# Kernel optimization log

Hardware: AMD Instinct MI355X
Metric: run time of the kernel (lower is better)

The kernel has to match this reference:

```python
import jax, jax.numpy as jnp
import numpy as np

LAYERS = [2048, 2048, 2048, 512]
THRESHOLD = 1.0
TAU_MEM = 20.0
TAU_SYN = 5.0
DT = 1.0
BATCH = 32
T = 100


def setup_inputs() -> dict:
    key = jax.random.key(0)
    ks = jax.random.split(key, 2 + 2 * (len(LAYERS) - 1))
    inp = {
        "x": jax.random.uniform(ks[0], (BATCH, LAYERS[0]), dtype=jnp.float32),
        "noise": jax.random.uniform(ks[1], (T, BATCH, LAYERS[0]), dtype=jnp.float32),
        "time_steps": T,
    }
    # nn.Linear-style init: U(-1/sqrt(fan_in), 1/sqrt(fan_in))
    for i in range(len(LAYERS) - 1):
        fan_in, fan_out = LAYERS[i], LAYERS[i + 1]
        bound = 1.0 / np.sqrt(fan_in)
        inp[f"W{i}"] = jax.random.uniform(ks[2 + 2 * i], (fan_out, fan_in), minval=-bound, maxval=bound, dtype=jnp.float32)
        inp[f"b{i}"] = jax.random.uniform(ks[3 + 2 * i], (fan_out,), minval=-bound, maxval=bound, dtype=jnp.float32)
    return inp


def _lif_step(I, mem, syn):
    # dI_syn/dt = -I_syn/tau_syn + I ; dV/dt = -V/tau_mem + I_syn  (explicit Euler, dt=1)
    syn = syn + (-syn / TAU_SYN + I) * DT
    mem = mem + (-mem / TAU_MEM + syn) * DT
    spikes = (mem >= THRESHOLD).astype(mem.dtype)
    mem = mem * (1.0 - spikes)          # reset fired neurons
    mem = mem * (mem > 0).astype(mem.dtype)  # clamp negative potentials to 0
    return spikes, mem, syn


def reference(x, noise, W0, b0, W1, b1, W2, b2, time_steps):
    params = [(W0, b0), (W1, b1), (W2, b2)]
    batch = x.shape[0]
    dtype = x.dtype
    rate = jnp.clip(x, 0.0, 1.0)                       # [B, in]
    in_spikes = (noise < rate[None]).astype(dtype)     # [T, B, in] Poisson encoding

    mems = tuple(jnp.zeros((batch, W.shape[0]), dtype) for W, _ in params)
    syns = tuple(jnp.zeros((batch, W.shape[0]), dtype) for W, _ in params)

    def step(carry, sp_in):
        mems, syns = carry
        layer_in = sp_in
        new_mems, new_syns = [], []
        count = jnp.zeros((), dtype)
        for (W, b), m, s in zip(params, mems, syns):
            I = layer_in @ W.T + b
            spk, m, s = _lif_step(I, m, s)
            new_mems.append(m)
            new_syns.append(s)
            count = count + spk.sum()
            layer_in = spk
        return (tuple(new_mems), tuple(new_syns)), (layer_in, count)

    (_, _), (out_spikes, counts) = jax.lax.scan(step, (mems, syns), in_spikes)
    output = out_spikes.mean(axis=0)   # [B, out]: time-averaged output spike train
    total_spikes = counts.sum()
    return output, total_spikes
```

## Files before the change

kernel.cpp:

```cpp
#include <hip/hip_runtime.h>
#include <hip/hip_cooperative_groups.h>

#define T_STEPS 100
#define MTOT    3200
#define R0_OFF  0
#define R1_OFF  13107200
#define I_OFF   26214400

typedef _Float16 half8_t __attribute__((ext_vector_type(8)));
typedef _Float16 half4_t __attribute__((ext_vector_type(4)));
typedef float    f32x4   __attribute__((ext_vector_type(4)));

__device__ __forceinline__ void encode512_body(
    int blk, const float* __restrict__ x, const float* __restrict__ noise,
    _Float16* __restrict__ spk0, float* __restrict__ out, _Float16* smem)
{
    if (blk == 0 && threadIdx.x == 0) out[16384] = 0.0f;
    const int tid  = threadIdx.x;
    const int m0   = blk * 16;
    const int koct = tid & 255;
    const int mlh  = tid >> 8;
    half8_t* lds = (half8_t*)smem;
    #pragma unroll
    for (int mlq = 0; mlq < 8; ++mlq) {
        const int ml = mlq * 2 + mlh;
        const int m  = m0 + ml;
        const int t = m >> 5, b = m & 31;
        const float4 x1 = *(const float4*)(x + b * 2048 + koct * 8);
        const float4 x2 = *(const float4*)(x + b * 2048 + koct * 8 + 4);
        const float4 n1 = *(const float4*)(noise + (size_t)t * 65536 + b * 2048 + koct * 8);
        const float4 n2 = *(const float4*)(noise + (size_t)t * 65536 + b * 2048 + koct * 8 + 4);
        const float xr[8] = {x1.x,x1.y,x1.z,x1.w,x2.x,x2.y,x2.z,x2.w};
        const float nz[8] = {n1.x,n1.y,n1.z,n1.w,n2.x,n2.y,n2.z,n2.w};
        half8_t sp;
        #pragma unroll
        for (int q = 0; q < 8; ++q) {
            const float r = fminf(fmaxf(xr[q], 0.0f), 1.0f);
            sp[q] = (nz[q] < r) ? (_Float16)1.0f : (_Float16)0.0f;
        }
        lds[ml * 256 + (koct ^ ml)] = sp;
    }
    __syncthreads();
    #pragma unroll
    for (int r = 0; r < 8; ++r) {
        const int ml  = tid & 15;
        const int oct = r * 32 + (tid >> 4);
        *(half8_t*)(spk0 + ((size_t)oct * MTOT + m0 + ml) * 8)
            = lds[ml * 256 + (oct ^ ml)];
    }
}

__device__ __forceinline__ void convw512_body(
    int cblk, const float* __restrict__ W, _Float16* __restrict__ Wf)
{
    const int koct = threadIdx.x & 255;
    const int rh   = threadIdx.x >> 8;
    #pragma unroll
    for (int r = 0; r < 8; ++r) {
        const int row = cblk * 16 + rh * 8 + r;
        const float* wp = W + (size_t)row * 2048 + koct * 8;
        const float4 f1 = *(const float4*)(wp);
        const float4 f2 = *(const float4*)(wp + 4);
        half8_t h = {(_Float16)f1.x,(_Float16)f1.y,(_Float16)f1.z,(_Float16)f1.w,
                     (_Float16)f2.x,(_Float16)f2.y,(_Float16)f2.z,(_Float16)f2.w};
        const size_t idx = (size_t)(row >> 4) * 32768
                         + ((size_t)((koct >> 2) * 64 + (koct & 3) * 16 + (row & 15))) * 8;
        *(half8_t*)(Wf + idx) = h;
    }
}

__device__ __forceinline__ void scan512_body(
    int blk, const _Float16* __restrict__ I, const float* __restrict__ bias,
    _Float16* __restrict__ spk_out, float* __restrict__ out,
    const int is_last, float* rsum)
{
    const int gid = blk * 512 + threadIdx.x;
    const int j   = gid & 7;
    const int b   = (gid >> 3) & 31;
    const int oct = gid >> 8;
    const int n   = oct * 8 + j;
    const float bi = bias[n];
    const size_t nbase = (size_t)oct * (MTOT * 8) + j;
    float mem = 0.f, syn = 0.f, osum = 0.f, cnt = 0.f;
    #pragma unroll 4
    for (int t = 0; t < T_STEPS; ++t) {
        const int m = t * 32 + b;
        const float Iv = (float)I[nbase + (size_t)m * 8] + bi;
        syn = syn + (-syn / 5.0f + Iv);
        mem = mem + (-mem / 20.0f + syn);
        const float sv = (mem >= 1.0f) ? 1.0f : 0.0f;
        mem = (sv != 0.0f) ? 0.0f : mem;
        mem = (mem > 0.0f) ? mem : 0.0f;
        cnt += sv; osum += sv;
        if (!is_last) spk_out[nbase + (size_t)m * 8] = (_Float16)sv;
    }
    if (is_last) out[b * 512 + n] = osum * 0.01f;
    float c = cnt;
    #pragma unroll
    for (int s2 = 1; s2 < 64; s2 <<= 1) c += __shfl_xor(c, s2);
    const int wid = threadIdx.x >> 6;
    if ((threadIdx.x & 63) == 0) rsum[wid] = c;
    __syncthreads();
    if (threadIdx.x == 0) {
        float s = rsum[0];
        #pragma unroll
        for (int ww = 1; ww < 8; ++ww) s += rsum[ww];
        atomicAdd(&out[16384], s);
    }
    __syncthreads();
}

__device__ __forceinline__ half8_t ldB(const _Float16* __restrict__ p, int kq) {
    return *(const half8_t*)(p + (size_t)kq * (MTOT * 8));
}

__device__ __forceinline__ void stage_q(
    const _Float16* __restrict__ Wf, _Float16* __restrict__ wlds,
    const int nbb, const int q, const int w, const int lane)
{
    #pragma unroll
    for (int r = 0; r < 8; ++r) {
        const int unit = r * 512 + w * 64 + lane;
        const int s = unit >> 10, off = unit & 1023;
        const _Float16* src = Wf + (size_t)(4 * nbb + s) * 32768
                            + (size_t)q * 8192 + (size_t)off * 8;
        _Float16* dst = wlds + (size_t)unit * 8;
        __builtin_amdgcn_global_load_lds(
            (const __attribute__((address_space(1))) void*)src,
            (__attribute__((address_space(3))) void*)dst, 16, 0, 0);
    }
}

template<bool HAS2>
__device__ __forceinline__ void kstep512(
    const _Float16* __restrict__ wlds, const _Float16* const (&bp)[2],
    half8_t (&bb)[2], f32x4 (&acc)[2][4],
    const int lane, const int quad, const int kb, const int j)
{
    half8_t a[4];
    #pragma unroll
    for (int s = 0; s < 4; ++s)
        a[s] = *(const half8_t*)(wlds + (size_t)s * 8192 + (size_t)(j * 64 + lane) * 8);
    #pragma unroll
    for (int s = 0; s < 4; ++s) {
        acc[0][s] = __builtin_amdgcn_mfma_f32_16x16x32_f16(a[s], bb[0], acc[0][s], 0, 0, 0);
        if (HAS2)
            acc[1][s] = __builtin_amdgcn_mfma_f32_16x16x32_f16(a[s], bb[1], acc[1][s], 0, 0, 0);
    }
    if (kb + 4 < 64) {
        const int kq = (kb + 4) * 4 + quad;
        bb[0] = ldB(bp[0], kq);
        if (HAS2) bb[1] = ldB(bp[1], kq);
    }
}

template<bool HAS2>
__device__ __forceinline__ void gemm64s_run(
    const _Float16* __restrict__ Wf, const _Float16* __restrict__ spk,
    _Float16* __restrict__ I, _Float16* __restrict__ wlds,
    const int (&mt)[2], const int nbb, const int row_base,
    const int w, const int lane, const int quad, const int mi,
    const bool st)
{
    const _Float16* bp[2];
    bp[0] = spk + ((size_t)mt[0] * 16 + mi) * 8;
    bp[1] = spk + ((size_t)mt[1] * 16 + mi) * 8;

    half8_t B0[2], B1[2], B2[2], B3[2];
    B0[0] = ldB(bp[0],      quad);
    B1[0] = ldB(bp[0],  4 + quad);
    B2[0] = ldB(bp[0],  8 + quad);
    B3[0] = ldB(bp[0], 12 + quad);
    if (HAS2) {
        B0[1] = ldB(bp[1],      quad);
        B1[1] = ldB(bp[1],  4 + quad);
        B2[1] = ldB(bp[1],  8 + quad);
        B3[1] = ldB(bp[1], 12 + quad);
    }

    stage_q(Wf, wlds, nbb, 0, w, lane);
    __syncthreads();

    f32x4 acc[2][4];
    #pragma unroll
    for (int u = 0; u < 2; ++u) {
        #pragma unroll
        for (int s = 0; s < 4; ++s) acc[u][s] = (f32x4){0, 0, 0, 0};
    }

    #pragma unroll 1
    for (int q = 0; q < 4; ++q) {
        #pragma unroll
        for (int j = 0; j < 16; j += 4) {
            kstep512<HAS2>(wlds, bp, B0, acc, lane, quad, q * 16 + j,     j);
            kstep512<HAS2>(wlds, bp, B1, acc, lane, quad, q * 16 + j + 1, j + 1);
            kstep512<HAS2>(wlds, bp, B2, acc, lane, quad, q * 16 + j + 2, j + 2);
            kstep512<HAS2>(wlds, bp, B3, acc, lane, quad, q * 16 + j + 3, j + 3);
        }
        __syncthreads();
        if (q < 3) {
            stage_q(Wf, wlds, nbb, q + 1, w, lane);
            __syncthreads();
        }
    }

    #pragma unroll
    for (int s = 0; s < 4; ++s) {
        const int n0 = row_base + s * 16 + quad * 4;
        const size_t obase = (size_t)(n0 >> 3) * (MTOT * 8) + (n0 & 7);
        #pragma unroll
        for (int u = 0; u < 2; ++u) {
            if (u == 0 && !st) continue;
            if (u == 1 && !HAS2) continue;
            half4_t h;
            #pragma unroll
            for (int r = 0; r < 4; ++r) h[r] = (_Float16)acc[u][s][r];
            *(half4_t*)(I + obase + (size_t)(mt[u] * 16 + mi) * 8) = h;
        }
    }
}

template<int NCHUNK>
__device__ __forceinline__ void gemm64s_body(
    const int bid, const _Float16* __restrict__ Wf,
    const _Float16* __restrict__ spk, _Float16* __restrict__ I,
    _Float16* __restrict__ wlds)
{
    const int tid  = threadIdx.x;
    const int lane = tid & 63;
    const int w    = tid >> 6;
    const int mi   = lane & 15;
    const int quad = lane >> 4;
    const int chunk = bid % NCHUNK;
    const int rest  = bid / NCHUNK;
    const int msl   = rest & 1;
    const int nbb   = rest >> 1;
    const int row_base = nbb * 64;
    const int jt     = (200 - chunk + NCHUNK - 1) / NCHUNK;
    const int jh     = (jt + 1) >> 1;
    const int jbase  = msl ? jh : 0;
    const int jcount = msl ? (jt - jh) : jh;
    const int rem    = jcount - 8;
    const bool has2  = (w < rem);
    const int r2     = rem > 0 ? rem : 0;
    const bool st    = has2 || (w + r2) < jcount;
    int jl_start = jbase + (has2 ? 2 * w : w + r2);
    const int jmax = jbase + jcount - 1;
    if (jl_start > jmax) jl_start = jmax;

    int mt[2];
    #pragma unroll
    for (int u = 0; u < 2; ++u) {
        int jl = jl_start + u;
        if (jl > jmax) jl = jmax;
        mt[u] = chunk + NCHUNK * jl;
    }

    if (has2) gemm64s_run<true >(Wf, spk, I, wlds, mt, nbb, row_base, w, lane, quad, mi, true);
    else      gemm64s_run<false>(Wf, spk, I, wlds, mt, nbb, row_base, w, lane, quad, mi, st);
}

__global__ __launch_bounds__(512, 4) void snn_mega_kernel(
    const float* __restrict__ x, const float* __restrict__ noise,
    const float* __restrict__ W0, const float* __restrict__ b0,
    const float* __restrict__ W1, const float* __restrict__ b1,
    const float* __restrict__ W2, const float* __restrict__ b2,
    _Float16* __restrict__ R0, _Float16* __restrict__ R1,
    _Float16* __restrict__ Ib, float* __restrict__ out)
{
    cooperative_groups::grid_group grid = cooperative_groups::this_grid();
    __shared__ _Float16 smem[32768];
    const int blk = blockIdx.x;

    if (blk < 200)      encode512_body(blk, x, noise, R0, out, smem);
    else if (blk < 328) convw512_body(blk - 200, W0, R1);
    grid.sync();
    gemm64s_body<8>(blk, R1, R0, Ib, smem);
    grid.sync();
    if (blk < 128)      scan512_body(blk, Ib, b0, R1, out, 0, (float*)smem);
    else if (blk < 256) convw512_body(blk - 128, W1, R0);
    grid.sync();
    gemm64s_body<8>(blk, R0, R1, Ib, smem);
    grid.sync();
    if (blk < 128)      scan512_body(blk, Ib, b1, R0, out, 0, (float*)smem);
    else if (blk < 160) convw512_body(blk - 128, W2, R1);
    grid.sync();
    if (blk < 256) gemm64s_body<16>(blk, R1, R0, Ib, smem);
    grid.sync();
    if (blk < 32) scan512_body(blk, Ib, b2, nullptr, out, 1, (float*)smem);
}

__global__ __launch_bounds__(512, 4) void snn_enc512_kernel(
    const float* __restrict__ x, const float* __restrict__ noise,
    _Float16* __restrict__ spk0, float* __restrict__ out,
    const float* __restrict__ W, _Float16* __restrict__ Wf)
{
    __shared__ _Float16 smem[32768];
    if (blockIdx.x < 200) encode512_body(blockIdx.x, x, noise, spk0, out, smem);
    else                  convw512_body(blockIdx.x - 200, W, Wf);
}

__global__ __launch_bounds__(512, 4) void snn_scan_convw512_kernel(
    const _Float16* __restrict__ I, const float* __restrict__ bias,
    _Float16* __restrict__ spk_out, float* __restrict__ out,
    const int scan_blocks, const float* __restrict__ W,
    _Float16* __restrict__ Wf)
{
    __shared__ float rsum[8];
    if ((int)blockIdx.x < scan_blocks)
        scan512_body(blockIdx.x, I, bias, spk_out, out, 0, rsum);
    else
        convw512_body(blockIdx.x - scan_blocks, W, Wf);
}

__global__ __launch_bounds__(512, 4) void snn_scan512_kernel(
    const _Float16* __restrict__ I, const float* __restrict__ bias,
    float* __restrict__ out)
{
    __shared__ float rsum[8];
    scan512_body(blockIdx.x, I, bias, nullptr, out, 1, rsum);
}

template<int NCHUNK>
__global__ __launch_bounds__(512, 4) void snn_gemm64s_kernel(
    const _Float16* __restrict__ Wf, const _Float16* __restrict__ spk,
    _Float16* __restrict__ I)
{
    __shared__ _Float16 wlds[32768];
    gemm64s_body<NCHUNK>(blockIdx.x, Wf, spk, I, wlds);
}

extern "C" void kernel_launch(void* const* d_in, const int* in_sizes, int n_in,
                              void* d_out, int out_size, void* d_ws, size_t ws_size,
                              hipStream_t stream) {
    const float* x     = (const float*)d_in[0];
    const float* noise = (const float*)d_in[1];
    const float* W0 = (const float*)d_in[3];
    const float* b0 = (const float*)d_in[4];
    const float* W1 = (const float*)d_in[5];
    const float* b1 = (const float*)d_in[6];
    const float* W2 = (const float*)d_in[7];
    const float* b2 = (const float*)d_in[8];
    float* out = (float*)d_out;

    _Float16* R0 = (_Float16*)((char*)d_ws + R0_OFF);
    _Float16* R1 = (_Float16*)((char*)d_ws + R1_OFF);
    _Float16* Ib = (_Float16*)((char*)d_ws + I_OFF);

    int maxb = 0;
    hipError_t oe = hipOccupancyMaxActiveBlocksPerMultiprocessor(
        &maxb, (const void*)snn_mega_kernel, 512, 0);

    if (oe == hipSuccess && maxb >= 2) {
        void* args[] = {(void*)&x, (void*)&noise,
                        (void*)&W0, (void*)&b0, (void*)&W1, (void*)&b1,
                        (void*)&W2, (void*)&b2,
                        (void*)&R0, (void*)&R1, (void*)&Ib, (void*)&out};
        hipLaunchCooperativeKernel((const void*)snn_mega_kernel,
                                   dim3(512), dim3(512), args, 0, stream);
    } else {
        snn_enc512_kernel<<<dim3(328), dim3(512), 0, stream>>>(x, noise, R0, out, W0, R1);
        snn_gemm64s_kernel<8><<<dim3(512), dim3(512), 0, stream>>>(R1, R0, Ib);
        snn_scan_convw512_kernel<<<dim3(256), dim3(512), 0, stream>>>(Ib, b0, R1, out, 128, W1, R0);
        snn_gemm64s_kernel<8><<<dim3(512), dim3(512), 0, stream>>>(R0, R1, Ib);
        snn_scan_convw512_kernel<<<dim3(160), dim3(512), 0, stream>>>(Ib, b1, R0, out, 128, W2, R1);
        snn_gemm64s_kernel<16><<<dim3(256), dim3(512), 0, stream>>>(R1, R0, Ib);
        snn_scan512_kernel<<<dim3(32), dim3(512), 0, stream>>>(Ib, b2, out);
    }

    (void)in_sizes; (void)n_in; (void)out_size; (void)ws_size;
}
```

Before: 245.7 us.

## Replace cooperative grid.sync with custom sharded atomic barriers and MFMA priority hints

Swaps the six cooperative-groups grid syncs for a hand-rolled barrier that spreads arrival counters over 8 cache-line-separated slots and uses a per-launch invocation counter to derive monotonically increasing targets, so the counters never need resetting. It also raises wave priority around the MFMA block and adds empty asm register constraints to pin B-operand loads in place. The goal is lower barrier latency and better MFMA issue. The barrier relies on relaxed atomics plus fences and assumes exactly 512 resident blocks, which is fragile if the grid size changes.

```diff
diff --git a/kernel.cpp b/kernel.cpp
--- a/kernel.cpp
+++ b/kernel.cpp
@@ -10,6 +10,28 @@
 typedef _Float16 half8_t __attribute__((ext_vector_type(8)));
 typedef _Float16 half4_t __attribute__((ext_vector_type(4)));
 typedef float    f32x4   __attribute__((ext_vector_type(4)));
+
+__device__ int g_inv;
+__device__ __attribute__((aligned(1024))) int g_bar[6][128];
+
+__device__ __forceinline__ void gate(const int p, const int target) {
+    __syncthreads();
+    if (threadIdx.x == 0) {
+        __threadfence();
+        __hip_atomic_fetch_add(&g_bar[p][(blockIdx.x & 7) * 16], 1,
+                               __ATOMIC_RELAXED, __HIP_MEMORY_SCOPE_AGENT);
+    }
+    if (threadIdx.x < 8) {
+        while (__hip_atomic_load(&g_bar[p][threadIdx.x * 16],
+                                 __ATOMIC_RELAXED, __HIP_MEMORY_SCOPE_AGENT)
+               < target) {
+            __builtin_amdgcn_s_sleep(1);
+        }
+    }
+    __syncthreads();
+    __threadfence();
+    __syncthreads();
+}
 
 __device__ __forceinline__ void encode512_body(
     int blk, const float* __restrict__ x, const float* __restrict__ noise,
@@ -48,6 +70,7 @@
         *(half8_t*)(spk0 + ((size_t)oct * MTOT + m0 + ml) * 8)
             = lds[ml * 256 + (oct ^ ml)];
     }
+    __syncthreads();
 }
 
 __device__ __forceinline__ void convw512_body(
@@ -141,16 +164,22 @@
     #pragma unroll
     for (int s = 0; s < 4; ++s)
         a[s] = *(const half8_t*)(wlds + (size_t)s * 8192 + (size_t)(j * 64 + lane) * 8);
+    __builtin_amdgcn_s_setprio(1);
     #pragma unroll
     for (int s = 0; s < 4; ++s) {
         acc[0][s] = __builtin_amdgcn_mfma_f32_16x16x32_f16(a[s], bb[0], acc[0][s], 0, 0, 0);
         if (HAS2)
             acc[1][s] = __builtin_amdgcn_mfma_f32_16x16x32_f16(a[s], bb[1], acc[1][s], 0, 0, 0);
     }
+    __builtin_amdgcn_s_setprio(0);
     if (kb + 4 < 64) {
         const int kq = (kb + 4) * 4 + quad;
         bb[0] = ldB(bp[0], kq);
-        if (HAS2) bb[1] = ldB(bp[1], kq);
+        asm volatile("" : "+v"(bb[0]));
+        if (HAS2) {
+            bb[1] = ldB(bp[1], kq);
+            asm volatile("" : "+v"(bb[1]));
+        }
     }
 }
 
@@ -171,11 +200,13 @@
     B1[0] = ldB(bp[0],  4 + quad);
     B2[0] = ldB(bp[0],  8 + quad);
     B3[0] = ldB(bp[0], 12 + quad);
+    asm volatile("" : "+v"(B0[0]), "+v"(B1[0]), "+v"(B2[0]), "+v"(B3[0]));
     if (HAS2) {
         B0[1] = ldB(bp[1],      quad);
         B1[1] = ldB(bp[1],  4 + quad);
         B2[1] = ldB(bp[1],  8 + quad);
         B3[1] = ldB(bp[1], 12 + quad);
+        asm volatile("" : "+v"(B0[1]), "+v"(B1[1]), "+v"(B2[1]), "+v"(B3[1]));
     }
 
     stage_q(Wf, wlds, nbb, 0, w, lane);
@@ -268,25 +299,33 @@
     _Float16* __restrict__ R0, _Float16* __restrict__ R1,
     _Float16* __restrict__ Ib, float* __restrict__ out)
 {
-    cooperative_groups::grid_group grid = cooperative_groups::this_grid();
     __shared__ _Float16 smem[32768];
+    __shared__ int s_k;
     const int blk = blockIdx.x;
+
+    if (threadIdx.x == 0) {
+        const int v = __hip_atomic_fetch_add(&g_inv, 1, __ATOMIC_RELAXED,
+                                             __HIP_MEMORY_SCOPE_AGENT);
+        s_k = (v >> 9) + 1;
+    }
+    __syncthreads();
+    const int tgt = 64 * s_k;
 
     if (blk < 200)      encode512_body(blk, x, noise, R0, out, smem);
     else if (blk < 328) convw512_body(blk - 200, W0, R1);
-    grid.sync();
+    gate(0, tgt);
     gemm64s_body<8>(blk, R1, R0, Ib, smem);
-    grid.sync();
+    gate(1, tgt);
     if (blk < 128)      scan512_body(blk, Ib, b0, R1, out, 0, (float*)smem);
     else if (blk < 256) convw512_body(blk - 128, W1, R0);
-    grid.sync();
+    gate(2, tgt);
     gemm64s_body<8>(blk, R0, R1, Ib, smem);
-    grid.sync();
+    gate(3, tgt);
     if (blk < 128)      scan512_body(blk, Ib, b1, R0, out, 0, (float*)smem);
     else if (blk < 160) convw512_body(blk - 128, W2, R1);
-    grid.sync();
+    gate(4, tgt);
     if (blk < 256) gemm64s_body<16>(blk, R1, R0, Ib, smem);
-    grid.sync();
+    gate(5, tgt);
     if (blk < 32) scan512_body(blk, Ib, b2, nullptr, out, 1, (float*)smem);
 }
 
```

Measured after the change: 298.3 us. 1.21x slower.

## Convert all weights upfront and prestage next-layer weights into LDS during scan

Applied to the files above, without the earlier changes.

When the workspace is large enough, the W1 and W2 fp32-to-fp16 conversions move into the first phase, using otherwise idle blocks and separate workspace buffers. During each scan phase, every block also preloads its first quarter of the next layer's weight tile into LDS, so the following GEMM skips its initial staging load and barrier. The aim is to take the weight-conversion work and the first LDS fill off the critical path between grid syncs. The cost is more workspace memory and a dependence on ws_size, and the scan's use of shared memory has to coexist with the prestaged tile in the same LDS buffer.

```diff
diff --git a/kernel.cpp b/kernel.cpp
--- a/kernel.cpp
+++ b/kernel.cpp
@@ -6,6 +6,9 @@
 #define R0_OFF  0
 #define R1_OFF  13107200
 #define I_OFF   26214400
+#define W1F_OFF 39321600
+#define W2F_OFF 47710208
+#define WS_CONS 49807360ULL
 
 typedef _Float16 half8_t __attribute__((ext_vector_type(8)));
 typedef _Float16 half4_t __attribute__((ext_vector_type(4)));
@@ -48,6 +51,7 @@
         *(half8_t*)(spk0 + ((size_t)oct * MTOT + m0 + ml) * 8)
             = lds[ml * 256 + (oct ^ ml)];
     }
+    __syncthreads();
 }
 
 __device__ __forceinline__ void convw512_body(
@@ -154,7 +158,7 @@
     }
 }
 
-template<bool HAS2>
+template<bool HAS2, bool PRE>
 __device__ __forceinline__ void gemm64s_run(
     const _Float16* __restrict__ Wf, const _Float16* __restrict__ spk,
     _Float16* __restrict__ I, _Float16* __restrict__ wlds,
@@ -178,8 +182,10 @@
         B3[1] = ldB(bp[1], 12 + quad);
     }
 
-    stage_q(Wf, wlds, nbb, 0, w, lane);
-    __syncthreads();
+    if (!PRE) {
+        stage_q(Wf, wlds, nbb, 0, w, lane);
+        __syncthreads();
+    }
 
     f32x4 acc[2][4];
     #pragma unroll
@@ -220,7 +226,7 @@
     }
 }
 
-template<int NCHUNK>
+template<int NCHUNK, bool PRE>
 __device__ __forceinline__ void gemm64s_body(
     const int bid, const _Float16* __restrict__ Wf,
     const _Float16* __restrict__ spk, _Float16* __restrict__ I,
@@ -256,8 +262,8 @@
         mt[u] = chunk + NCHUNK * jl;
     }
 
-    if (has2) gemm64s_run<true >(Wf, spk, I, wlds, mt, nbb, row_base, w, lane, quad, mi, true);
-    else      gemm64s_run<false>(Wf, spk, I, wlds, mt, nbb, row_base, w, lane, quad, mi, st);
+    if (has2) gemm64s_run<true , PRE>(Wf, spk, I, wlds, mt, nbb, row_base, w, lane, quad, mi, true);
+    else      gemm64s_run<false, PRE>(Wf, spk, I, wlds, mt, nbb, row_base, w, lane, quad, mi, st);
 }
 
 __global__ __launch_bounds__(512, 4) void snn_mega_kernel(
@@ -266,26 +272,45 @@
     const float* __restrict__ W1, const float* __restrict__ b1,
     const float* __restrict__ W2, const float* __restrict__ b2,
     _Float16* __restrict__ R0, _Float16* __restrict__ R1,
-    _Float16* __restrict__ Ib, float* __restrict__ out)
+    _Float16* __restrict__ Ib, _Float16* __restrict__ W1F,
+    _Float16* __restrict__ W2F, const int cons,
+    float* __restrict__ out)
 {
     cooperative_groups::grid_group grid = cooperative_groups::this_grid();
     __shared__ _Float16 smem[32768];
     const int blk = blockIdx.x;
+    const int w = threadIdx.x >> 6, lane = threadIdx.x & 63;
 
     if (blk < 200)      encode512_body(blk, x, noise, R0, out, smem);
     else if (blk < 328) convw512_body(blk - 200, W0, R1);
-    grid.sync();
-    gemm64s_body<8>(blk, R1, R0, Ib, smem);
-    grid.sync();
-    if (blk < 128)      scan512_body(blk, Ib, b0, R1, out, 0, (float*)smem);
-    else if (blk < 256) convw512_body(blk - 128, W1, R0);
-    grid.sync();
-    gemm64s_body<8>(blk, R0, R1, Ib, smem);
-    grid.sync();
-    if (blk < 128)      scan512_body(blk, Ib, b1, R0, out, 0, (float*)smem);
-    else if (blk < 160) convw512_body(blk - 128, W2, R1);
-    grid.sync();
-    if (blk < 256) gemm64s_body<16>(blk, R1, R0, Ib, smem);
+    else if (cons && blk < 456) convw512_body(blk - 328, W1, W1F);
+    else if (cons && blk < 488) convw512_body(blk - 456, W2, W2F);
+    grid.sync();
+    gemm64s_body<8, false>(blk, R1, R0, Ib, smem);
+    grid.sync();
+    if (cons) {
+        if (blk < 128) scan512_body(blk, Ib, b0, R1, out, 0, (float*)smem);
+        stage_q(W1F, smem, (blk >> 3) >> 1, 0, w, lane);
+    } else {
+        if (blk < 128)      scan512_body(blk, Ib, b0, R1, out, 0, (float*)smem);
+        else if (blk < 256) convw512_body(blk - 128, W1, R0);
+    }
+    grid.sync();
+    if (cons) gemm64s_body<8, true >(blk, W1F, R1, Ib, smem);
+    else      gemm64s_body<8, false>(blk, R0,  R1, Ib, smem);
+    grid.sync();
+    if (cons) {
+        if (blk < 128) scan512_body(blk, Ib, b1, R0, out, 0, (float*)smem);
+        if (blk < 256) stage_q(W2F, smem, (blk >> 4) >> 1, 0, w, lane);
+    } else {
+        if (blk < 128)      scan512_body(blk, Ib, b1, R0, out, 0, (float*)smem);
+        else if (blk < 160) convw512_body(blk - 128, W2, R1);
+    }
+    grid.sync();
+    if (blk < 256) {
+        if (cons) gemm64s_body<16, true >(blk, W2F, R0, Ib, smem);
+        else      gemm64s_body<16, false>(blk, R1,  R0, Ib, smem);
+    }
     grid.sync();
     if (blk < 32) scan512_body(blk, Ib, b2, nullptr, out, 1, (float*)smem);
 }
@@ -327,7 +352,7 @@
     _Float16* __restrict__ I)
 {
     __shared__ _Float16 wlds[32768];
-    gemm64s_body<NCHUNK>(blockIdx.x, Wf, spk, I, wlds);
+    gemm64s_body<NCHUNK, false>(blockIdx.x, Wf, spk, I, wlds);
 }
 
 extern "C" void kernel_launch(void* const* d_in, const int* in_sizes, int n_in,
@@ -346,6 +371,9 @@
     _Float16* R0 = (_Float16*)((char*)d_ws + R0_OFF);
     _Float16* R1 = (_Float16*)((char*)d_ws + R1_OFF);
     _Float16* Ib = (_Float16*)((char*)d_ws + I_OFF);
+    const int cons = (ws_size >= WS_CONS) ? 1 : 0;
+    _Float16* W1F = cons ? (_Float16*)((char*)d_ws + W1F_OFF) : R0;
+    _Float16* W2F = cons ? (_Float16*)((char*)d_ws + W2F_OFF) : R0;
 
     int maxb = 0;
     hipError_t oe = hipOccupancyMaxActiveBlocksPerMultiprocessor(
@@ -355,7 +383,9 @@
         void* args[] = {(void*)&x, (void*)&noise,
                         (void*)&W0, (void*)&b0, (void*)&W1, (void*)&b1,
                         (void*)&W2, (void*)&b2,
-                        (void*)&R0, (void*)&R1, (void*)&Ib, (void*)&out};
+                        (void*)&R0, (void*)&R1, (void*)&Ib,
+                        (void*)&W1F, (void*)&W2F, (void*)&cons,
+                        (void*)&out};
         hipLaunchCooperativeKernel((const void*)snn_mega_kernel,
                                    dim3(512), dim3(512), args, 0, stream);
     } else {
```

Result: no change. 250.2 us (+1.8%).

## Rebalance per-stage work across all 512 cooperative blocks

Applied to the files above, without the earlier changes.

Splits encode into 8-row blocks (400 blocks), makes weight conversion do 32 rows per block, halves scan work per block so 256 blocks participate, and generalizes the GEMM M-split so the last layer GEMM uses all 512 blocks with a 4-way split. The aim is to use more CUs in each phase between grid syncs instead of leaving many blocks idle. In exchange, half the threads in scan blocks sit idle and conversion blocks carry more serial work.

```diff
diff --git a/kernel.cpp b/kernel.cpp
--- a/kernel.cpp
+++ b/kernel.cpp
@@ -11,18 +11,18 @@
 typedef _Float16 half4_t __attribute__((ext_vector_type(4)));
 typedef float    f32x4   __attribute__((ext_vector_type(4)));
 
-__device__ __forceinline__ void encode512_body(
+__device__ __forceinline__ void encode8_body(
     int blk, const float* __restrict__ x, const float* __restrict__ noise,
     _Float16* __restrict__ spk0, float* __restrict__ out, _Float16* smem)
 {
     if (blk == 0 && threadIdx.x == 0) out[16384] = 0.0f;
     const int tid  = threadIdx.x;
-    const int m0   = blk * 16;
+    const int m0   = blk * 8;
     const int koct = tid & 255;
     const int mlh  = tid >> 8;
     half8_t* lds = (half8_t*)smem;
     #pragma unroll
-    for (int mlq = 0; mlq < 8; ++mlq) {
+    for (int mlq = 0; mlq < 4; ++mlq) {
         const int ml = mlq * 2 + mlh;
         const int m  = m0 + ml;
         const int t = m >> 5, b = m & 31;
@@ -42,22 +42,23 @@
     }
     __syncthreads();
     #pragma unroll
-    for (int r = 0; r < 8; ++r) {
-        const int ml  = tid & 15;
-        const int oct = r * 32 + (tid >> 4);
+    for (int r = 0; r < 4; ++r) {
+        const int ml  = tid & 7;
+        const int oct = r * 64 + (tid >> 3);
         *(half8_t*)(spk0 + ((size_t)oct * MTOT + m0 + ml) * 8)
             = lds[ml * 256 + (oct ^ ml)];
     }
-}
-
-__device__ __forceinline__ void convw512_body(
+    __syncthreads();
+}
+
+__device__ __forceinline__ void convw32_body(
     int cblk, const float* __restrict__ W, _Float16* __restrict__ Wf)
 {
     const int koct = threadIdx.x & 255;
     const int rh   = threadIdx.x >> 8;
     #pragma unroll
-    for (int r = 0; r < 8; ++r) {
-        const int row = cblk * 16 + rh * 8 + r;
+    for (int r = 0; r < 16; ++r) {
+        const int row = cblk * 32 + rh * 16 + r;
         const float* wp = W + (size_t)row * 2048 + koct * 8;
         const float4 f1 = *(const float4*)(wp);
         const float4 f2 = *(const float4*)(wp + 4);
@@ -69,32 +70,35 @@
     }
 }
 
-__device__ __forceinline__ void scan512_body(
+__device__ __forceinline__ void scan256_body(
     int blk, const _Float16* __restrict__ I, const float* __restrict__ bias,
     _Float16* __restrict__ spk_out, float* __restrict__ out,
     const int is_last, float* rsum)
 {
-    const int gid = blk * 512 + threadIdx.x;
-    const int j   = gid & 7;
-    const int b   = (gid >> 3) & 31;
-    const int oct = gid >> 8;
-    const int n   = oct * 8 + j;
-    const float bi = bias[n];
-    const size_t nbase = (size_t)oct * (MTOT * 8) + j;
-    float mem = 0.f, syn = 0.f, osum = 0.f, cnt = 0.f;
-    #pragma unroll 4
-    for (int t = 0; t < T_STEPS; ++t) {
-        const int m = t * 32 + b;
-        const float Iv = (float)I[nbase + (size_t)m * 8] + bi;
-        syn = syn + (-syn / 5.0f + Iv);
-        mem = mem + (-mem / 20.0f + syn);
-        const float sv = (mem >= 1.0f) ? 1.0f : 0.0f;
-        mem = (sv != 0.0f) ? 0.0f : mem;
-        mem = (mem > 0.0f) ? mem : 0.0f;
-        cnt += sv; osum += sv;
-        if (!is_last) spk_out[nbase + (size_t)m * 8] = (_Float16)sv;
-    }
-    if (is_last) out[b * 512 + n] = osum * 0.01f;
+    float cnt = 0.f;
+    if (threadIdx.x < 256) {
+        const int gid = blk * 256 + threadIdx.x;
+        const int j   = gid & 7;
+        const int b   = (gid >> 3) & 31;
+        const int oct = gid >> 8;
+        const int n   = oct * 8 + j;
+        const float bi = bias[n];
+        const size_t nbase = (size_t)oct * (MTOT * 8) + j;
+        float mem = 0.f, syn = 0.f, osum = 0.f;
+        #pragma unroll 10
+        for (int t = 0; t < T_STEPS; ++t) {
+            const int m = t * 32 + b;
+            const float Iv = (float)I[nbase + (size_t)m * 8] + bi;
+            syn = syn + (-syn / 5.0f + Iv);
+            mem = mem + (-mem / 20.0f + syn);
+            const float sv = (mem >= 1.0f) ? 1.0f : 0.0f;
+            mem = (sv != 0.0f) ? 0.0f : mem;
+            mem = (mem > 0.0f) ? mem : 0.0f;
+            cnt += sv; osum += sv;
+            if (!is_last) spk_out[nbase + (size_t)m * 8] = (_Float16)sv;
+        }
+        if (is_last) out[b * 512 + n] = osum * 0.01f;
+    }
     float c = cnt;
     #pragma unroll
     for (int s2 = 1; s2 < 64; s2 <<= 1) c += __shfl_xor(c, s2);
@@ -220,7 +224,7 @@
     }
 }
 
-template<int NCHUNK>
+template<int NCHUNK, int MSPLIT>
 __device__ __forceinline__ void gemm64s_body(
     const int bid, const _Float16* __restrict__ Wf,
     const _Float16* __restrict__ spk, _Float16* __restrict__ I,
@@ -233,13 +237,12 @@
     const int quad = lane >> 4;
     const int chunk = bid % NCHUNK;
     const int rest  = bid / NCHUNK;
-    const int msl   = rest & 1;
-    const int nbb   = rest >> 1;
+    const int msl   = rest % MSPLIT;
+    const int nbb   = rest / MSPLIT;
     const int row_base = nbb * 64;
     const int jt     = (200 - chunk + NCHUNK - 1) / NCHUNK;
-    const int jh     = (jt + 1) >> 1;
-    const int jbase  = msl ? jh : 0;
-    const int jcount = msl ? (jt - jh) : jh;
+    const int jbase  = (jt * msl) / MSPLIT;
+    const int jcount = (jt * (msl + 1)) / MSPLIT - jbase;
     const int rem    = jcount - 8;
     const bool has2  = (w < rem);
     const int r2     = rem > 0 ? rem : 0;
@@ -272,22 +275,22 @@
     __shared__ _Float16 smem[32768];
     const int blk = blockIdx.x;
 
-    if (blk < 200)      encode512_body(blk, x, noise, R0, out, smem);
-    else if (blk < 328) convw512_body(blk - 200, W0, R1);
-    grid.sync();
-    gemm64s_body<8>(blk, R1, R0, Ib, smem);
-    grid.sync();
-    if (blk < 128)      scan512_body(blk, Ib, b0, R1, out, 0, (float*)smem);
-    else if (blk < 256) convw512_body(blk - 128, W1, R0);
-    grid.sync();
-    gemm64s_body<8>(blk, R0, R1, Ib, smem);
-    grid.sync();
-    if (blk < 128)      scan512_body(blk, Ib, b1, R0, out, 0, (float*)smem);
-    else if (blk < 160) convw512_body(blk - 128, W2, R1);
-    grid.sync();
-    if (blk < 256) gemm64s_body<16>(blk, R1, R0, Ib, smem);
-    grid.sync();
-    if (blk < 32) scan512_body(blk, Ib, b2, nullptr, out, 1, (float*)smem);
+    if (blk < 400)      encode8_body(blk, x, noise, R0, out, smem);
+    else if (blk < 464) convw32_body(blk - 400, W0, R1);
+    grid.sync();
+    gemm64s_body<8, 2>(blk, R1, R0, Ib, smem);
+    grid.sync();
+    if (blk < 256)      scan256_body(blk, Ib, b0, R1, out, 0, (float*)smem);
+    else if (blk < 320) convw32_body(blk - 256, W1, R0);
+    grid.sync();
+    gemm64s_body<8, 2>(blk, R0, R1, Ib, smem);
+    grid.sync();
+    if (blk < 256)      scan256_body(blk, Ib, b1, R0, out, 0, (float*)smem);
+    else if (blk < 272) convw32_body(blk - 256, W2, R1);
+    grid.sync();
+    gemm64s_body<16, 4>(blk, R1, R0, Ib, smem);
+    grid.sync();
+    if (blk < 64) scan256_body(blk, Ib, b2, nullptr, out, 1, (float*)smem);
 }
 
 __global__ __launch_bounds__(512, 4) void snn_enc512_kernel(
@@ -296,8 +299,8 @@
     const float* __restrict__ W, _Float16* __restrict__ Wf)
 {
     __shared__ _Float16 smem[32768];
-    if (blockIdx.x < 200) encode512_body(blockIdx.x, x, noise, spk0, out, smem);
-    else                  convw512_body(blockIdx.x - 200, W, Wf);
+    if (blockIdx.x < 400) encode8_body(blockIdx.x, x, noise, spk0, out, smem);
+    else                  convw32_body(blockIdx.x - 400, W, Wf);
 }
 
 __global__ __launch_bounds__(512, 4) void snn_scan_convw512_kernel(
@@ -308,9 +311,9 @@
 {
     __shared__ float rsum[8];
     if ((int)blockIdx.x < scan_blocks)
-        scan512_body(blockIdx.x, I, bias, spk_out, out, 0, rsum);
+        scan256_body(blockIdx.x, I, bias, spk_out, out, 0, rsum);
     else
-        convw512_body(blockIdx.x - scan_blocks, W, Wf);
+        convw32_body(blockIdx.x - scan_blocks, W, Wf);
 }
 
 __global__ __launch_bounds__(512, 4) void snn_scan512_kernel(
@@ -318,16 +321,16 @@
     float* __restrict__ out)
 {
     __shared__ float rsum[8];
-    scan512_body(blockIdx.x, I, bias, nullptr, out, 1, rsum);
-}
-
-template<int NCHUNK>
+    scan256_body(blockIdx.x, I, bias, nullptr, out, 1, rsum);
+}
+
+template<int NCHUNK, int MSPLIT>
 __global__ __launch_bounds__(512, 4) void snn_gemm64s_kernel(
     const _Float16* __restrict__ Wf, const _Float16* __restrict__ spk,
     _Float16* __restrict__ I)
 {
     __shared__ _Float16 wlds[32768];
-    gemm64s_body<NCHUNK>(blockIdx.x, Wf, spk, I, wlds);
+    gemm64s_body<NCHUNK, MSPLIT>(blockIdx.x, Wf, spk, I, wlds);
 }
 
 extern "C" void kernel_launch(void* const* d_in, const int* in_sizes, int n_in,
@@ -359,13 +362,13 @@
         hipLaunchCooperativeKernel((const void*)snn_mega_kernel,
                                    dim3(512), dim3(512), args, 0, stream);
     } else {
-        snn_enc512_kernel<<<dim3(328), dim3(512), 0, stream>>>(x, noise, R0, out, W0, R1);
-        snn_gemm64s_kernel<8><<<dim3(512), dim3(512), 0, stream>>>(R1, R0, Ib);
-        snn_scan_convw512_kernel<<<dim3(256), dim3(512), 0, stream>>>(Ib, b0, R1, out, 128, W1, R0);
-        snn_gemm64s_kernel<8><<<dim3(512), dim3(512), 0, stream>>>(R0, R1, Ib);
-        snn_scan_convw512_kernel<<<dim3(160), dim3(512), 0, stream>>>(Ib, b1, R0, out, 128, W2, R1);
-        snn_gemm64s_kernel<16><<<dim3(256), dim3(512), 0, stream>>>(R1, R0, Ib);
-        snn_scan512_kernel<<<dim3(32), dim3(512), 0, stream>>>(Ib, b2, out);
+        snn_enc512_kernel<<<dim3(464), dim3(512), 0, stream>>>(x, noise, R0, out, W0, R1);
+        snn_gemm64s_kernel<8, 2><<<dim3(512), dim3(512), 0, stream>>>(R1, R0, Ib);
+        snn_scan_convw512_kernel<<<dim3(320), dim3(512), 0, stream>>>(Ib, b0, R1, out, 256, W1, R0);
+        snn_gemm64s_kernel<8, 2><<<dim3(512), dim3(512), 0, stream>>>(R0, R1, Ib);
+        snn_scan_convw512_kernel<<<dim3(272), dim3(512), 0, stream>>>(Ib, b1, R0, out, 256, W2, R1);
+        snn_gemm64s_kernel<16, 4><<<dim3(512), dim3(512), 0, stream>>>(R1, R0, Ib);
+        snn_scan512_kernel<<<dim3(64), dim3(512), 0, stream>>>(Ib, b2, out);
     }
 
     (void)in_sizes; (void)n_in; (void)out_size; (void)ws_size;
```

Result: slower. 257.4 us (+4.8%).
